# Kernel tuning notes

Measured on AMD Instinct MI355X. Metric: run time of the kernel, lower is better.

The kernel has to match this reference:

```python
import jax, jax.numpy as jnp
import numpy as np

B, T, D, H = 32, 512, 1024, 16
HD = D // H  # 64


def setup_inputs() -> dict:
    key = jax.random.key(0)
    ks = jax.random.split(key, 12)
    s_in = 1.0 / np.sqrt(D)
    x = jax.random.normal(ks[0], (B, T, D), dtype=jnp.float32)
    Wi = jax.random.normal(ks[1], (D, D), dtype=jnp.float32) * s_in
    bi = jnp.zeros((D,), dtype=jnp.float32)
    Wk = jax.random.normal(ks[2], (H, D, HD), dtype=jnp.float32) * s_in
    bk = jnp.zeros((H, HD), dtype=jnp.float32)
    Wq = jax.random.normal(ks[3], (H, D, HD), dtype=jnp.float32) * s_in
    bq = jnp.zeros((H, HD), dtype=jnp.float32)
    Wv = jax.random.normal(ks[4], (H, D, HD), dtype=jnp.float32) * s_in
    bv = jnp.zeros((H, HD), dtype=jnp.float32)
    Wo = jax.random.normal(ks[5], (D, D), dtype=jnp.float32) * s_in
    bo = jnp.zeros((D,), dtype=jnp.float32)
    return {"x": x, "Wi": Wi, "bi": bi, "Wk": Wk, "bk": bk,
            "Wq": Wq, "bq": bq, "Wv": Wv, "bv": bv, "Wo": Wo, "bo": bo}


def reference(x, Wi, bi, Wk, bk, Wq, bq, Wv, bv, Wo, bo):
    # in_proj
    h = x @ Wi + bi  # [B,T,D]
    # per-head K/Q/V projections, vectorized over heads
    k = jnp.einsum('btd,hde->bhte', h, Wk) + bk[None, :, None, :]  # [B,H,T,HD]
    q = jnp.einsum('btd,hde->bhte', h, Wq) + bq[None, :, None, :]
    v = jnp.einsum('btd,hde->bhte', h, Wv) + bv[None, :, None, :]
    # NOTE: original computes wei = k @ q^T (keys as rows), masks with tril,
    # softmax over last axis (queries). Faithfully reproduced (no scaling).
    wei = jnp.einsum('bhtd,bhsd->bhts', k, q)  # [B,H,T,T]
    causal = jnp.tril(jnp.ones((T, T), dtype=bool))
    wei = jnp.where(causal, wei, -jnp.inf)
    wei = jax.nn.softmax(wei, axis=-1)
    # dropout: eval mode (identity)
    out = jnp.einsum('bhts,bhsd->bhtd', wei, v)  # [B,H,T,HD]
    out = out.transpose(0, 2, 1, 3).reshape(B, T, D)  # concat heads on last dim
    return out @ Wo + bo
```

## Files before the change

kernel.cpp:

```cpp
#include <hip/hip_runtime.h>
#include <hip/hip_bf16.h>
#include <stdint.h>

#define NTOK 16384

typedef _Float16 f16;
typedef f16   f16x8 __attribute__((ext_vector_type(8)));
typedef float f32x4 __attribute__((ext_vector_type(4)));

__device__ __forceinline__ float bf2f(ushort h){
  union { uint32_t u; float f; } v; v.u = ((uint32_t)h) << 16; return v.f;
}
__device__ __forceinline__ ushort f2bf(float f){
  union { float f; uint32_t u; } v; v.f = f;
  uint32_t u = v.u;
  return (ushort)((u + 0x7FFFu + ((u >> 16) & 1u)) >> 16);
}
__device__ __forceinline__ ushort f2h(float f){
  return __builtin_bit_cast(ushort, (f16)f);
}
__device__ __forceinline__ f16x8 ld16(const ushort* p){
  uint4 u = *(const uint4*)p;
  return __builtin_bit_cast(f16x8, u);
}
__device__ __forceinline__ float ldf(const void* p, size_t idx, int isf32){
  if (isf32) return ((const float*)p)[idx];
  return bf2f(((const ushort*)p)[idx]);
}

__device__ __forceinline__ const ushort* swz(const ushort* base, uint row, uint chunk){
  return base + (size_t)row*64u + (size_t)((chunk ^ (row & 7u))*8u);
}

__device__ __forceinline__ void stage64(const ushort* g, uint strideEl,
                                        ushort* ldsbase, uint tid){
  uint w = tid >> 6;
  #pragma unroll
  for (int i = 0; i < 2; ++i){
    uint lc  = i*256u + tid;
    uint row = lc >> 3, cp = lc & 7u;
    uint c   = cp ^ (row & 7u);
    const ushort* gp = g + (size_t)row*strideEl + c*8u;
    ushort* lp = ldsbase + (size_t)(i*256u + w*64u)*8u;
    __builtin_amdgcn_global_load_lds((const __attribute__((address_space(1))) void*)gp,
        (__attribute__((address_space(3))) void*)lp, 16, 0, 0);
  }
}

__device__ __forceinline__ void stage128(const ushort* g, int K,
                                         ushort* ldsbase, uint tid){
  uint w = tid >> 6;
  #pragma unroll
  for (int i = 0; i < 4; ++i){
    uint lc  = i*256u + tid;
    uint row = lc >> 3, cp = lc & 7u;
    uint c   = cp ^ (row & 7u);
    const ushort* gp = g + (size_t)row*(size_t)K + c*8u;
    ushort* lp = ldsbase + (size_t)(i*256u + w*64u)*8u;
    __builtin_amdgcn_global_load_lds((const __attribute__((address_space(1))) void*)gp,
        (__attribute__((address_space(3))) void*)lp, 16, 0, 0);
  }
}

__global__ __launch_bounds__(256) void kprep(const void* __restrict__ x,
                                             const void* __restrict__ Wi, const void* __restrict__ Wo,
                                             const void* __restrict__ Wk, const void* __restrict__ Wq,
                                             const void* __restrict__ Wv,
                                             const void* __restrict__ bi, const void* __restrict__ bo,
                                             const void* __restrict__ bk, const void* __restrict__ bq,
                                             const void* __restrict__ bv,
                                             int* __restrict__ flag,
                                             float* __restrict__ bi_f, float* __restrict__ bo_f,
                                             float* __restrict__ bqkv_f,
                                             ushort* __restrict__ xh, ushort* __restrict__ WiT,
                                             ushort* __restrict__ WoT, ushort* __restrict__ WqkvT){
  __shared__ int cnt_s;
  __shared__ float tile[64][65];
  uint t = threadIdx.x, q = blockIdx.x;
  if (t == 0) cnt_s = 0;
  __syncthreads();
  {
    uint wv = ((const uint*)Wi)[t];
    uint e = (wv >> 7) & 0xFFu;
    if (e >= 100u && e <= 130u) atomicAdd(&cnt_s, 1);
  }
  __syncthreads();
  int f = (cnt_s < 128) ? 1 : 0;

  if (q < 8192u){
    size_t g = (size_t)(q*256u + t)*8u;
    ushort o[8];
    if (f){
      const float4* xf = (const float4*)((const float*)x + g);
      float4 a = xf[0], b2 = xf[1];
      o[0] = f2h(a.x);  o[1] = f2h(a.y);  o[2] = f2h(a.z);  o[3] = f2h(a.w);
      o[4] = f2h(b2.x); o[5] = f2h(b2.y); o[6] = f2h(b2.z); o[7] = f2h(b2.w);
    } else {
      uint4 u = *(const uint4*)((const ushort*)x + g);
      ushort s[8];
      *(uint4*)s = u;
      #pragma unroll
      for (int i = 0; i < 8; ++i) o[i] = f2h(bf2f(s[i]));
    }
    *(uint4*)(xh + g) = *(uint4*)o;
  } else if (q < 8704u){
    uint qq = q - 8192u;
    const void* in = (qq < 256u) ? Wi : Wo;
    ushort* out = (qq < 256u) ? WiT : WoT;
    uint qi = qq & 255u;
    uint R0 = (qi & 15u)*64u, C0 = (qi >> 4)*64u;
    #pragma unroll
    for (int i = 0; i < 16; ++i){
      uint id = i*256u + t, r = id >> 6, c = id & 63u;
      tile[r][c] = ldf(in, (size_t)(R0 + r)*1024u + C0 + c, f);
    }
    __syncthreads();
    #pragma unroll
    for (int i = 0; i < 16; ++i){
      uint id = i*256u + t, r = id >> 6, c = id & 63u;
      out[(size_t)(C0 + r)*1024u + R0 + c] = f2h(tile[c][r]);
    }
  } else if (q < 9472u){
    uint qq = q - 8704u;
    uint sh = qq % 48u, D0 = (qq / 48u)*64u;
    uint sel = sh >> 4, h = sh & 15u;
    const void* W = (sel == 0) ? Wk : ((sel == 1) ? Wq : Wv);
    #pragma unroll
    for (int i = 0; i < 16; ++i){
      uint id = i*256u + t, r = id >> 6, c = id & 63u;
      tile[r][c] = ldf(W, (size_t)h*65536u + (size_t)(D0 + r)*64u + c, f);
    }
    __syncthreads();
    #pragma unroll
    for (int i = 0; i < 16; ++i){
      uint id = i*256u + t, r = id >> 6, c = id & 63u;
      WqkvT[(size_t)(sel*1024u + h*64u + r)*1024u + D0 + c] = f2h(tile[c][r]);
    }
  } else {
    uint id = (q - 9472u)*256u + t;
    if (id < 1024u)       bi_f[id]         = ldf(bi, id, f);
    else if (id < 2048u)  bo_f[id - 1024u] = ldf(bo, id - 1024u, f);
    else {
      uint j = id - 2048u;
      uint sel = j >> 10, i = j & 1023u;
      const void* src = (sel == 0) ? bk : ((sel == 1) ? bq : bv);
      bqkv_f[j] = ldf(src, i, f);
    }
    if (q == 9472u && t == 0) flag[0] = f;
  }
}

template<int MODE>
__global__ __launch_bounds__(256, 4) void kgemm(const ushort* __restrict__ A, const ushort* __restrict__ Bt,
                                                const float* __restrict__ bias, void* __restrict__ Cv,
                                                ushort* __restrict__ Vt, const int* __restrict__ dtf,
                                                int M, int N, int K, int cb){
  __shared__ ushort sA[128*64];
  __shared__ ushort sB[128*64];
  uint tid = threadIdx.x, w = tid >> 6, lane = tid & 63u, quad = lane >> 4, l15 = lane & 15u;
  uint bm = blockIdx.x, bn = blockIdx.y;
  uint wm = w >> 1, wn = w & 1u;
  f32x4 acc[4][4] = {};

  for (int k0 = 0; k0 < K; k0 += 64){
    stage128(A  + (size_t)(bm*128u)*(size_t)K + k0, K, sA, tid);
    stage128(Bt + (size_t)(bn*128u)*(size_t)K + k0, K, sB, tid);
    __syncthreads();
    #pragma unroll
    for (int kk = 0; kk < 2; ++kk){
      f16x8 aF[4], bF[4];
      #pragma unroll
      for (int i = 0; i < 4; ++i) aF[i] = ld16(swz(sA, wm*64u + (uint)i*16u + l15, (uint)kk*4u + quad));
      #pragma unroll
      for (int j = 0; j < 4; ++j) bF[j] = ld16(swz(sB, wn*64u + (uint)j*16u + l15, (uint)kk*4u + quad));
      #pragma unroll
      for (int i = 0; i < 4; ++i)
        #pragma unroll
        for (int j = 0; j < 4; ++j)
          acc[i][j] = __builtin_amdgcn_mfma_f32_16x16x32_f16(aF[i], bF[j], acc[i][j], 0, 0, 0);
    }
    __syncthreads();
  }
  int f32out = (MODE == 2) ? dtf[0] : 0;
  const float L2E = 1.44269504088896340736f;
  #pragma unroll
  for (int j = 0; j < 4; ++j){
    uint col = bn*128u + wn*64u + j*16u + l15;
    float bj = bias[col];
    #pragma unroll
    for (int i = 0; i < 4; ++i){
      uint row0 = bm*128u + wm*64u + i*16u + quad*4u;
      #pragma unroll
      for (int r = 0; r < 4; ++r){
        float val = acc[i][j][r] + bj;
        uint row = row0 + r;
        if (MODE == 0){
          ((ushort*)Cv)[(size_t)row*N + col] = f2h(val);
        } else if (MODE == 3){
          float v2 = cb ? val * L2E : val;
          ((ushort*)Cv)[(size_t)row*2048u + (uint)cb + col] = f2h(v2);
        } else if (MODE == 4){
          Vt[(size_t)(((row >> 9)*16u + (col >> 6))*64u + (col & 63u))*512u + (row & 511u)] = f2h(val);
        } else {
          if (f32out) ((float*)Cv)[(size_t)row*N + col] = val;
          else        ((ushort*)Cv)[(size_t)row*N + col] = f2bf(val);
        }
      }
    }
  }
}

__global__ __launch_bounds__(256, 4) void kattn(const ushort* __restrict__ kq,
                                                const ushort* __restrict__ Vt,
                                                ushort* __restrict__ Out){
  __shared__ ushort sQ[2][64*64];
  __shared__ ushort sV[2][64*64];
  __shared__ ushort pbuf[4][16*64];
  uint tid = threadIdx.x, w = tid >> 6, lane = tid & 63u, quad = lane >> 4, l15 = lane & 15u;
  uint bh = blockIdx.x, tt = 7u - blockIdx.y;
  uint b = bh >> 4, h = bh & 15u;
  uint t0 = tt*64u;
  const float MNEG = -1.0e30f;

  stage64(kq + (size_t)(b*512u + t0)*2048u + h*64u, 2048u, (ushort*)pbuf, tid);
  stage64(kq + (size_t)(b*512u)*2048u + 1024u + h*64u, 2048u, sQ[0], tid);
  stage64(Vt + (size_t)(bh*64u)*512u, 512u, sV[0], tid);
  __syncthreads();

  f16x8 aK[2];
  aK[0] = ld16(swz((const ushort*)pbuf, w*16u + l15, quad));
  aK[1] = ld16(swz((const ushort*)pbuf, w*16u + l15, 4u + quad));

  float m[4], l[4];
  f32x4 oacc[4];
  #pragma unroll
  for (int r = 0; r < 4; ++r){ m[r] = MNEG; l[r] = 0.f; }
  #pragma unroll
  for (int je = 0; je < 4; ++je) oacc[je] = (f32x4){0.f, 0.f, 0.f, 0.f};

  ushort* pw = (ushort*)pbuf + w*1024u;

  for (uint st = 0; st <= tt; ++st){
    uint cur = st & 1u;
    if (st) __syncthreads();
    if (st < tt){
      uint s1 = (st + 1u)*64u;
      stage64(kq + (size_t)(b*512u + s1)*2048u + 1024u + h*64u, 2048u, sQ[1u - cur], tid);
      stage64(Vt + (size_t)(bh*64u)*512u + s1, 512u, sV[1u - cur], tid);
    }
    f32x4 sacc[4];
    #pragma unroll
    for (int j = 0; j < 4; ++j){
      f16x8 bq0 = ld16(swz(sQ[cur], j*16u + l15, quad));
      f16x8 bq1 = ld16(swz(sQ[cur], j*16u + l15, 4u + quad));
      f32x4 s = (f32x4){0.f, 0.f, 0.f, 0.f};
      s = __builtin_amdgcn_mfma_f32_16x16x32_f16(aK[0], bq0, s, 0, 0, 0);
      s = __builtin_amdgcn_mfma_f32_16x16x32_f16(aK[1], bq1, s, 0, 0, 0);
      sacc[j] = s;
    }
    if (st == tt){
      #pragma unroll
      for (int j = 0; j < 4; ++j)
        #pragma unroll
        for (int r = 0; r < 4; ++r)
          if (j*16u + l15 > w*16u + quad*4u + (uint)r) sacc[j][r] = MNEG;
    }
    float alpha[4];
    #pragma unroll
    for (int r = 0; r < 4; ++r){
      float v = fmaxf(fmaxf(sacc[0][r], sacc[1][r]), fmaxf(sacc[2][r], sacc[3][r]));
      v = fmaxf(v, __shfl_xor(v, 1));
      v = fmaxf(v, __shfl_xor(v, 2));
      v = fmaxf(v, __shfl_xor(v, 4));
      v = fmaxf(v, __shfl_xor(v, 8));
      float mn = fmaxf(m[r], v);
      alpha[r] = exp2f(m[r] - mn);
      m[r] = mn;
    }
    #pragma unroll
    for (int j = 0; j < 4; ++j)
      #pragma unroll
      for (int r = 0; r < 4; ++r)
        sacc[j][r] = exp2f(sacc[j][r] - m[r]);
    #pragma unroll
    for (int r = 0; r < 4; ++r){
      float s = sacc[0][r] + sacc[1][r] + sacc[2][r] + sacc[3][r];
      s += __shfl_xor(s, 1);
      s += __shfl_xor(s, 2);
      s += __shfl_xor(s, 4);
      s += __shfl_xor(s, 8);
      l[r] = l[r]*alpha[r] + s;
    }
    #pragma unroll
    for (int je = 0; je < 4; ++je)
      #pragma unroll
      for (int r = 0; r < 4; ++r)
        oacc[je][r] *= alpha[r];
    #pragma unroll
    for (int j = 0; j < 4; ++j)
      #pragma unroll
      for (int r = 0; r < 4; ++r){
        uint t = quad*4u + (uint)r;
        pw[t*64u + (((j*2u + (l15 >> 3)) ^ (t & 7u))*8u) + (l15 & 7u)] = f2h(sacc[j][r]);
      }
    f16x8 aP0 = ld16(swz(pw, l15, quad));
    f16x8 aP1 = ld16(swz(pw, l15, 4u + quad));
    #pragma unroll
    for (int je = 0; je < 4; ++je){
      f16x8 bv0 = ld16(swz(sV[cur], je*16u + l15, quad));
      f16x8 bv1 = ld16(swz(sV[cur], je*16u + l15, 4u + quad));
      oacc[je] = __builtin_amdgcn_mfma_f32_16x16x32_f16(aP0, bv0, oacc[je], 0, 0, 0);
      oacc[je] = __builtin_amdgcn_mfma_f32_16x16x32_f16(aP1, bv1, oacc[je], 0, 0, 0);
    }
  }
  float inv[4];
  #pragma unroll
  for (int r = 0; r < 4; ++r) inv[r] = 1.0f / l[r];
  #pragma unroll
  for (int je = 0; je < 4; ++je){
    uint e = h*64u + je*16u + l15;
    #pragma unroll
    for (int r = 0; r < 4; ++r){
      uint t = t0 + w*16u + quad*4u + (uint)r;
      Out[(size_t)(b*512u + t)*1024u + e] = f2h(oacc[je][r]*inv[r]);
    }
  }
}


extern "C" void kernel_launch(void* const* d_in, const int* in_sizes, int n_in,
                              void* d_out, int out_size, void* d_ws, size_t ws_size,
                              hipStream_t stream){
  const void* x  = d_in[0];
  const void* Wi = d_in[1];
  const void* bi = d_in[2];
  const void* Wk = d_in[3];
  const void* bk = d_in[4];
  const void* Wq = d_in[5];
  const void* bq = d_in[6];
  const void* Wv = d_in[7];
  const void* bv = d_in[8];
  const void* Wo = d_in[9];
  const void* bo = d_in[10];
  char* ws = (char*)d_ws;

  const size_t MB = 1u << 20;
  int*    flag   = (int*)ws;
  float*  bi_f   = (float*)(ws + 4096);
  float*  bo_f   = (float*)(ws + 8192);
  float*  bqkv_f = (float*)(ws + 12288);
  ushort* WiT    = (ushort*)(ws + 32768);
  ushort* WoT    = (ushort*)(ws + 32768 + 2*MB);
  ushort* WqkvT  = (ushort*)(ws + 32768 + 4*MB);
  ushort* xh     = (ushort*)(ws + 32768 + 10*MB);
  ushort* kq     = (ushort*)(ws + 32768 + 10*MB);
  ushort* hbuf   = (ushort*)(ws + 32768 + 74*MB);
  ushort* Vt     = (ushort*)(ws + 32768 + 106*MB);

  kprep<<<dim3(9492), dim3(256), 0, stream>>>(x, Wi, Wo, Wk, Wq, Wv, bi, bo, bk, bq, bv,
                                              flag, bi_f, bo_f, bqkv_f, xh, WiT, WoT, WqkvT);

  kgemm<0><<<dim3(128, 8), dim3(256), 0, stream>>>(xh,   WiT, bi_f, hbuf, nullptr, nullptr, NTOK, 1024, 1024, 0);
  kgemm<3><<<dim3(128, 8), dim3(256), 0, stream>>>(hbuf, WqkvT,                      bqkv_f,        kq, nullptr, nullptr, NTOK, 1024, 1024, 0);
  kgemm<3><<<dim3(128, 8), dim3(256), 0, stream>>>(hbuf, WqkvT + (size_t)1024*1024,  bqkv_f + 1024, kq, nullptr, nullptr, NTOK, 1024, 1024, 1024);
  kgemm<4><<<dim3(128, 8), dim3(256), 0, stream>>>(hbuf, WqkvT + (size_t)2048*1024,  bqkv_f + 2048, nullptr, Vt, nullptr, NTOK, 1024, 1024, 0);
  kattn<<<dim3(512, 8), dim3(256), 0, stream>>>(kq, Vt, hbuf);
  kgemm<2><<<dim3(128, 8), dim3(256), 0, stream>>>(hbuf, WoT, bo_f, d_out, nullptr, flag, NTOK, 1024, 1024, 0);
}
```

Measured before the change: 443.1 us.

## Double-buffer GEMM K-loop and merge QKV projections into one launch

```diff
diff --git a/kernel.cpp b/kernel.cpp
--- a/kernel.cpp
+++ b/kernel.cpp
@@ -30,6 +30,10 @@
 
 __device__ __forceinline__ const ushort* swz(const ushort* base, uint row, uint chunk){
   return base + (size_t)row*64u + (size_t)((chunk ^ (row & 7u))*8u);
+}
+
+__device__ __forceinline__ const ushort* swz32(const ushort* base, uint row, uint chunk){
+  return base + (size_t)row*32u + (size_t)((chunk ^ ((row >> 1) & 3u))*8u);
 }
 
 __device__ __forceinline__ void stage64(const ushort* g, uint strideEl,
@@ -47,14 +51,14 @@
   }
 }
 
-__device__ __forceinline__ void stage128(const ushort* g, int K,
-                                         ushort* ldsbase, uint tid){
+__device__ __forceinline__ void stage32(const ushort* g, int K,
+                                        ushort* ldsbase, uint tid){
   uint w = tid >> 6;
   #pragma unroll
-  for (int i = 0; i < 4; ++i){
+  for (int i = 0; i < 2; ++i){
     uint lc  = i*256u + tid;
-    uint row = lc >> 3, cp = lc & 7u;
-    uint c   = cp ^ (row & 7u);
+    uint row = lc >> 2, cp = lc & 3u;
+    uint c   = cp ^ ((row >> 1) & 3u);
     const ushort* gp = g + (size_t)row*(size_t)K + c*8u;
     ushort* lp = ldsbase + (size_t)(i*256u + w*64u)*8u;
     __builtin_amdgcn_global_load_lds((const __attribute__((address_space(1))) void*)gp,
@@ -82,7 +86,8 @@
   {
     uint wv = ((const uint*)Wi)[t];
     uint e = (wv >> 7) & 0xFFu;
-    if (e >= 100u && e <= 130u) atomicAdd(&cnt_s, 1);
+    unsigned long long mask = __ballot(e >= 100u && e <= 130u);
+    if ((t & 63u) == 0u) atomicAdd(&cnt_s, __popcll(mask));
   }
   __syncthreads();
   int f = (cnt_s < 128) ? 1 : 0;
@@ -154,33 +159,40 @@
 __global__ __launch_bounds__(256, 4) void kgemm(const ushort* __restrict__ A, const ushort* __restrict__ Bt,
                                                 const float* __restrict__ bias, void* __restrict__ Cv,
                                                 ushort* __restrict__ Vt, const int* __restrict__ dtf,
-                                                int M, int N, int K, int cb){
-  __shared__ ushort sA[128*64];
-  __shared__ ushort sB[128*64];
+                                                int M, int N, int K){
+  __shared__ ushort sA[2][128*32];
+  __shared__ ushort sB[2][128*32];
   uint tid = threadIdx.x, w = tid >> 6, lane = tid & 63u, quad = lane >> 4, l15 = lane & 15u;
   uint bm = blockIdx.x, bn = blockIdx.y;
   uint wm = w >> 1, wn = w & 1u;
   f32x4 acc[4][4] = {};
 
-  for (int k0 = 0; k0 < K; k0 += 64){
-    stage128(A  + (size_t)(bm*128u)*(size_t)K + k0, K, sA, tid);
-    stage128(Bt + (size_t)(bn*128u)*(size_t)K + k0, K, sB, tid);
+  const ushort* GA = A  + (size_t)(bm*128u)*(size_t)K;
+  const ushort* GB = Bt + (size_t)(bn*128u)*(size_t)K;
+  const int NK = K >> 5;
+
+  stage32(GA, K, sA[0], tid);
+  stage32(GB, K, sB[0], tid);
+
+  for (int t = 0; t < NK; ++t){
+    uint bu = (uint)t & 1u;
     __syncthreads();
-    #pragma unroll
-    for (int kk = 0; kk < 2; ++kk){
-      f16x8 aF[4], bF[4];
-      #pragma unroll
-      for (int i = 0; i < 4; ++i) aF[i] = ld16(swz(sA, wm*64u + (uint)i*16u + l15, (uint)kk*4u + quad));
-      #pragma unroll
-      for (int j = 0; j < 4; ++j) bF[j] = ld16(swz(sB, wn*64u + (uint)j*16u + l15, (uint)kk*4u + quad));
-      #pragma unroll
-      for (int i = 0; i < 4; ++i)
-        #pragma unroll
-        for (int j = 0; j < 4; ++j)
-          acc[i][j] = __builtin_amdgcn_mfma_f32_16x16x32_f16(aF[i], bF[j], acc[i][j], 0, 0, 0);
-    }
-    __syncthreads();
-  }
+    if (t + 1 < NK){
+      stage32(GA + (size_t)(t + 1)*32u, K, sA[bu ^ 1u], tid);
+      stage32(GB + (size_t)(t + 1)*32u, K, sB[bu ^ 1u], tid);
+    }
+    f16x8 aF[4], bF[4];
+    #pragma unroll
+    for (int i = 0; i < 4; ++i) aF[i] = ld16(swz32(sA[bu], wm*64u + (uint)i*16u + l15, quad));
+    #pragma unroll
+    for (int j = 0; j < 4; ++j) bF[j] = ld16(swz32(sB[bu], wn*64u + (uint)j*16u + l15, quad));
+    #pragma unroll
+    for (int i = 0; i < 4; ++i)
+      #pragma unroll
+      for (int j = 0; j < 4; ++j)
+        acc[i][j] = __builtin_amdgcn_mfma_f32_16x16x32_f16(aF[i], bF[j], acc[i][j], 0, 0, 0);
+  }
+
   int f32out = (MODE == 2) ? dtf[0] : 0;
   const float L2E = 1.44269504088896340736f;
   #pragma unroll
@@ -196,11 +208,15 @@
         uint row = row0 + r;
         if (MODE == 0){
           ((ushort*)Cv)[(size_t)row*N + col] = f2h(val);
-        } else if (MODE == 3){
-          float v2 = cb ? val * L2E : val;
-          ((ushort*)Cv)[(size_t)row*2048u + (uint)cb + col] = f2h(v2);
-        } else if (MODE == 4){
-          Vt[(size_t)(((row >> 9)*16u + (col >> 6))*64u + (col & 63u))*512u + (row & 511u)] = f2h(val);
+        } else if (MODE == 1){
+          if (col < 1024u){
+            ((ushort*)Cv)[(size_t)row*2048u + col] = f2h(val);
+          } else if (col < 2048u){
+            ((ushort*)Cv)[(size_t)row*2048u + col] = f2h(val * L2E);
+          } else {
+            uint c2 = col - 2048u;
+            Vt[(size_t)(((row >> 9)*16u + (c2 >> 6))*64u + (c2 & 63u))*512u + (row & 511u)] = f2h(val);
+          }
         } else {
           if (f32out) ((float*)Cv)[(size_t)row*N + col] = val;
           else        ((ushort*)Cv)[(size_t)row*N + col] = f2bf(val);
@@ -360,10 +376,8 @@
   kprep<<<dim3(9492), dim3(256), 0, stream>>>(x, Wi, Wo, Wk, Wq, Wv, bi, bo, bk, bq, bv,
                                               flag, bi_f, bo_f, bqkv_f, xh, WiT, WoT, WqkvT);
 
-  kgemm<0><<<dim3(128, 8), dim3(256), 0, stream>>>(xh,   WiT, bi_f, hbuf, nullptr, nullptr, NTOK, 1024, 1024, 0);
-  kgemm<3><<<dim3(128, 8), dim3(256), 0, stream>>>(hbuf, WqkvT,                      bqkv_f,        kq, nullptr, nullptr, NTOK, 1024, 1024, 0);
-  kgemm<3><<<dim3(128, 8), dim3(256), 0, stream>>>(hbuf, WqkvT + (size_t)1024*1024,  bqkv_f + 1024, kq, nullptr, nullptr, NTOK, 1024, 1024, 1024);
-  kgemm<4><<<dim3(128, 8), dim3(256), 0, stream>>>(hbuf, WqkvT + (size_t)2048*1024,  bqkv_f + 2048, nullptr, Vt, nullptr, NTOK, 1024, 1024, 0);
+  kgemm<0><<<dim3(128, 8),  dim3(256), 0, stream>>>(xh,   WiT,   bi_f,   hbuf,  nullptr, nullptr, NTOK, 1024, 1024);
+  kgemm<1><<<dim3(128, 24), dim3(256), 0, stream>>>(hbuf, WqkvT, bqkv_f, kq,    Vt,      nullptr, NTOK, 3072, 1024);
   kattn<<<dim3(512, 8), dim3(256), 0, stream>>>(kq, Vt, hbuf);
-  kgemm<2><<<dim3(128, 8), dim3(256), 0, stream>>>(hbuf, WoT, bo_f, d_out, nullptr, flag, NTOK, 1024, 1024, 0);
-}
+  kgemm<2><<<dim3(128, 8),  dim3(256), 0, stream>>>(hbuf, WoT,   bo_f,   d_out, nullptr, flag,   NTOK, 1024, 1024);
+}
```

Result: slower. 479.6 us (+8.3%).
